# Performance work log

Measured on AMD Instinct MI355X. Metric: run time of the kernel, lower is better.

The kernel has to match this reference:

```python
import jax, jax.numpy as jnp
import numpy as np

N_NODES = 20000
N_EDGES = 160000
FEAT = 512
HEADS = 4
NEG_SLOPE = 0.2


def setup_inputs() -> dict:
    key = jax.random.key(0)
    ks = jax.random.split(key, 8)
    s = 1.0 / np.sqrt(FEAT)
    return {
        "x": jax.random.normal(ks[0], (N_NODES, FEAT), dtype=jnp.float32),
        "edge_index": jax.random.randint(ks[1], (2, N_EDGES), 0, N_NODES, dtype=jnp.int32),
        "W_l": jax.random.normal(ks[2], (FEAT, HEADS * FEAT), dtype=jnp.float32) * s,
        "W_r": jax.random.normal(ks[3], (FEAT, HEADS * FEAT), dtype=jnp.float32) * s,
        "att": jax.random.normal(ks[4], (HEADS, FEAT), dtype=jnp.float32) * s,
        "bias": jax.random.normal(ks[5], (FEAT,), dtype=jnp.float32) * 0.01,
        "W_cls": jax.random.normal(ks[6], (FEAT, 2), dtype=jnp.float32) * s,
        "b_cls": jnp.zeros((2,), dtype=jnp.float32),
    }


def reference(x, edge_index, W_l, W_r, att, bias, W_cls, b_cls):
    N = x.shape[0]
    H, C = att.shape
    # PyG GATv2Conv default: add self-loops
    loops = jnp.arange(N, dtype=edge_index.dtype)
    ei = jnp.concatenate([edge_index, jnp.stack([loops, loops])], axis=1)
    src, dst = ei[0], ei[1]  # message j -> i

    xl = (x @ W_l).reshape(N, H, C)  # source transform
    xr = (x @ W_r).reshape(N, H, C)  # target transform

    # GATv2 score: e_ij = att . LeakyReLU(xl_j + xr_i)   -> [E, H]
    u = xl[src] + xr[dst]                      # [E, H, C]
    e = jnp.einsum('ehc,hc->eh', jax.nn.leaky_relu(u, NEG_SLOPE), att)

    # segment softmax over incoming edges of each dst node
    m = jax.ops.segment_max(e, dst, num_segments=N)          # [N, H]
    alpha = jnp.exp(e - m[dst])
    denom = jax.ops.segment_sum(alpha, dst, num_segments=N)  # [N, H]
    alpha = alpha / denom[dst]

    # aggregate: out_i = sum_j alpha_ij * xl_j
    out = jax.ops.segment_sum(alpha[:, :, None] * xl[src], dst, num_segments=N)  # [N,H,C]
    out = out.mean(axis=1) + bias  # concat=False -> mean over heads, then bias

    return out @ W_cls + b_cls  # [N, num_classes]
```

## Files before the change

### kernel.cpp

```cpp
#include <hip/hip_runtime.h>
#include <hip/hip_bf16.h>

#define FEAT    512
#define HEADS   4
#define NEG     0.2f

typedef unsigned int uint;
typedef unsigned short ushort_t;
typedef __attribute__((ext_vector_type(8))) short bf16x8v;
typedef __attribute__((ext_vector_type(4))) float f32x4v;
typedef __attribute__((address_space(3))) uint lds_u32_t;
typedef __attribute__((address_space(1))) const uint g_u32_t;

__device__ inline float bf2f(ushort_t h) { return __uint_as_float(((uint)h) << 16); }
__device__ inline ushort_t f2bf(float f) {
    uint u = __float_as_uint(f);
    u += 0x7fff + ((u >> 16) & 1);
    return (ushort_t)(u >> 16);
}
__device__ inline float2 up2(uint d) {
    return make_float2(__uint_as_float(d << 16), __uint_as_float(d & 0xffff0000u));
}
__device__ inline float2 f2add(float2 a, float2 b) { return make_float2(a.x + b.x, a.y + b.y); }
__device__ inline float2 f2min0(float2 a) { return make_float2(fminf(a.x, 0.f), fminf(a.y, 0.f)); }
__device__ inline float2 f2fma(float2 a, float2 b, float2 c) {
    return make_float2(fmaf(a.x, b.x, c.x), fmaf(a.y, b.y, c.y));
}
__device__ inline float2 f2fmas(float s, float2 b, float2 c) {
    return make_float2(fmaf(s, b.x, c.x), fmaf(s, b.y, c.y));
}

__global__ __launch_bounds__(256) void prep_kernel(
    const ushort_t* __restrict__ xprobe, int* flag,
    int* __restrict__ deg, int N, int NBZ,
    const void* a0, ushort_t* o0, int n0, const void* a1, ushort_t* o1, int n1,
    const void* a2, ushort_t* o2, int n2, const void* a3, ushort_t* o3, int n3,
    const void* __restrict__ xin, ushort_t* __restrict__ xc, long long nx) {
    __shared__ int s_isbf;
    int tid = threadIdx.x;
    if (tid < 64) {
        int hits = 0;
        for (int i = tid; i < 128; i += 64) {
            ushort_t w = xprobe[2 * i];
            uint hb = (w >> 8) & 0x7f;
            hits += (hb >= 0x38 && hb <= 0x42) ? 1 : 0;
        }
        #pragma unroll
        for (int off = 32; off >= 1; off >>= 1) hits += __shfl_xor(hits, off);
        if (tid == 0) s_isbf = (hits >= 64) ? 1 : 0;
    }
    __syncthreads();
    int isbf = s_isbf;
    int b = blockIdx.x;
    if (b == 0 && tid == 0) *flag = isbf;

    if (b < NBZ) {
        int i0 = (b * 256 + tid) * 4;
        if (i0 + 4 <= N) *(int4*)&deg[i0] = make_int4(0, 0, 0, 0);
        else for (int j = 0; j < 4; ++j) if (i0 + j < N) deg[i0 + j] = 0;
        return;
    }
    if (b < NBZ + 15) {
        int idx = (b - NBZ) * 256 + tid;
        const void* srcs[4] = {a0, a1, a2, a3};
        ushort_t* dsts[4] = {o0, o1, o2, o3};
        int ns[4] = {n0, n1, n2, n3};
        #pragma unroll
        for (int k = 0; k < 4; ++k) {
            if (idx < ns[k]) {
                dsts[k][idx] = isbf ? ((const ushort_t*)srcs[k])[idx]
                                    : f2bf(((const float*)srcs[k])[idx]);
                return;
            }
            idx -= ns[k];
        }
        return;
    }
    if (isbf) return;
    long long i0 = ((long long)(b - NBZ - 15) * 256 + tid) * 8;
    if (i0 + 8 <= nx) {
        const float* f = (const float*)xin + i0;
        float4 a = *(const float4*)f, bb = *(const float4*)(f + 4);
        ushort_t o[8] = {f2bf(a.x), f2bf(a.y), f2bf(a.z), f2bf(a.w),
                         f2bf(bb.x), f2bf(bb.y), f2bf(bb.z), f2bf(bb.w)};
        *(uint4*)&xc[i0] = *(uint4*)o;
    } else {
        for (long long i = i0; i < nx; ++i) xc[i] = f2bf(((const float*)xin)[i]);
    }
}

__global__ void hist_kernel(const int* __restrict__ dst, int* deg, int E, int N) {
    int i = blockIdx.x * blockDim.x + threadIdx.x;
    if (i < E) {
        int d = dst[i];
        if ((uint)d < (uint)N) atomicAdd(&deg[d], 1);
    }
}

__global__ __launch_bounds__(256) void scan1(const int* __restrict__ deg, int* __restrict__ part,
                                             int* __restrict__ bsum, int N) {
    __shared__ int tmp[256];
    int b = blockIdx.x, tid = threadIdx.x;
    int i0 = b * 1024 + tid * 4;
    int v[4] = {0, 0, 0, 0};
    if (i0 + 4 <= N) { int4 q = *(const int4*)&deg[i0]; v[0]=q.x+1; v[1]=q.y+1; v[2]=q.z+1; v[3]=q.w+1; }
    else { for (int j = 0; j < 4; ++j) v[j] = (i0 + j < N) ? deg[i0 + j] + 1 : 0; }
    int s0 = v[0], s1 = s0 + v[1], s2 = s1 + v[2], s3 = s2 + v[3];
    tmp[tid] = s3;
    __syncthreads();
    for (int off = 1; off < 256; off <<= 1) {
        int t = (tid >= off) ? tmp[tid - off] : 0;
        __syncthreads();
        tmp[tid] += t;
        __syncthreads();
    }
    int base = tid ? tmp[tid - 1] : 0;
    int e[4] = {base, base + s0, base + s1, base + s2};
    if (i0 + 4 <= N) { *(int4*)&part[i0] = make_int4(e[0], e[1], e[2], e[3]); }
    else { for (int j = 0; j < 4; ++j) if (i0 + j < N) part[i0 + j] = e[j]; }
    if (tid == 255) bsum[b] = tmp[255];
}

__global__ __launch_bounds__(256) void scan3(const int* __restrict__ part, const int* __restrict__ bsum,
                                             int* __restrict__ offsets, int* __restrict__ cursor,
                                             int N, int Nb) {
    __shared__ int s_add, s_tot;
    int b = blockIdx.x, tid = threadIdx.x;
    if (tid < 64) {
        int v = (tid < Nb) ? bsum[tid] : 0;
        int incl = v;
        #pragma unroll
        for (int off = 1; off < 64; off <<= 1) {
            int t = __shfl_up(incl, off);
            if (tid >= off) incl += t;
        }
        if (tid == b) s_add = incl - v;
        if (tid == Nb - 1) s_tot = incl;
    }
    __syncthreads();
    int add = s_add;
    int i0 = b * 1024 + tid * 4;
    #pragma unroll
    for (int j = 0; j < 4; ++j) {
        int i = i0 + j;
        if (i < N) { int o = part[i] + add; offsets[i] = o; cursor[i] = o; }
    }
    if (b == Nb - 1 && tid == 0) offsets[N] = s_tot;
}

__global__ void scatter_kernel(const int* __restrict__ src, const int* __restrict__ dst,
                               int* cursor, int* srcs, int E, int N) {
    int i = blockIdx.x * blockDim.x + threadIdx.x;
    if (i >= E + N) return;
    int s, d;
    if (i < E) { s = src[i]; d = dst[i]; }
    else       { s = i - E; d = i - E; }
    if ((uint)d >= (uint)N) return;
    int pos = atomicAdd(&cursor[d], 1);
    if ((uint)pos < (uint)(E + N)) srcs[pos] = s;
}

__global__ __launch_bounds__(256) void transpose_canon2(const void* __restrict__ inL,
                                                        const void* __restrict__ inR,
                                                        ushort_t* __restrict__ outL,
                                                        ushort_t* __restrict__ outR,
                                                        const int* __restrict__ flag,
                                                        int K, int N) {
    __shared__ ushort_t t[64][72];
    const void* in = blockIdx.z ? inR : inL;
    ushort_t* outp = blockIdx.z ? outR : outL;
    int k0 = blockIdx.y * 64, n0 = blockIdx.x * 64;
    int tid = threadIdx.x;
    int r = tid >> 3;
    int c = (tid & 7) * 8;
    int isbf = *flag;
    #pragma unroll
    for (int p = 0; p < 2; ++p) {
        int row = r + p * 32;
        size_t base = (size_t)(k0 + row) * N + n0 + c;
        if (isbf) {
            *(uint4*)&t[row][c] = *(const uint4*)((const ushort_t*)in + base);
        } else {
            const float* f = (const float*)in + base;
            float4 a = *(const float4*)f, b = *(const float4*)(f + 4);
            ushort_t o[8] = {f2bf(a.x), f2bf(a.y), f2bf(a.z), f2bf(a.w),
                             f2bf(b.x), f2bf(b.y), f2bf(b.z), f2bf(b.w)};
            *(uint4*)&t[row][c] = *(uint4*)o;
        }
    }
    __syncthreads();
    #pragma unroll
    for (int p = 0; p < 2; ++p) {
        int row = r + p * 32;
        #pragma unroll
        for (int j = 0; j < 8; ++j)
            outp[(size_t)(n0 + row) * K + k0 + c + j] = t[c + j][row];
    }
}

__global__ __launch_bounds__(256) void gemm128(const ushort_t* A_bf, const ushort_t* A_cv,
                                               const int* __restrict__ flag,
                                               const ushort_t* __restrict__ Bt,
                                               ushort_t* __restrict__ C,
                                               int M, int Nn, int K) {
    constexpr int CSTR = 132;
    __shared__ ushort_t SH[128 * CSTR];
    ushort_t* As = SH;
    ushort_t* Bs = SH + 8192;
    const ushort_t* A = (*flag) ? A_bf : A_cv;
    int tid = threadIdx.x;
    int wave = tid >> 6, lane = tid & 63;
    int row0 = blockIdx.y * 128, col0 = blockIdx.x * 128;
    int wm = (wave >> 1) * 64, wn = (wave & 1) * 64;

    f32x4v acc[4][4];
    #pragma unroll
    for (int i = 0; i < 4; ++i)
        #pragma unroll
        for (int j = 0; j < 4; ++j) acc[i][j] = (f32x4v){0.f, 0.f, 0.f, 0.f};

    int fm = lane & 15, kq8 = (lane >> 4) * 8;

    const ushort_t* srcA[2]; ushort_t* dstA0[2]; ushort_t* dstA1[2];
    const ushort_t* srcB[2]; ushort_t* dstB0[2]; ushort_t* dstB1[2];
    #pragma unroll
    for (int i = 0; i < 2; ++i) {
        int p = (wave * 2 + i) * 64 + lane;
        int row = p >> 2, kp = p & 3;
        int gra = row0 + row; if (gra >= M) gra = M - 1;
        srcA[i] = &A[(size_t)gra * K + kp * 8];
        srcB[i] = &Bt[(size_t)(col0 + row) * K + kp * 8];
        dstA0[i] = &As[p * 8]; dstA1[i] = &As[4096 + p * 8];
        dstB0[i] = &Bs[p * 8]; dstB1[i] = &Bs[4096 + p * 8];
    }

    for (int k0 = 0; k0 < K; k0 += 64) {
        #pragma unroll
        for (int i = 0; i < 2; ++i) {
            __builtin_amdgcn_global_load_lds((g_u32_t*)srcA[i],        (lds_u32_t*)dstA0[i], 16, 0, 0);
            __builtin_amdgcn_global_load_lds((g_u32_t*)(srcA[i] + 32), (lds_u32_t*)dstA1[i], 16, 0, 0);
            __builtin_amdgcn_global_load_lds((g_u32_t*)srcB[i],        (lds_u32_t*)dstB0[i], 16, 0, 0);
            __builtin_amdgcn_global_load_lds((g_u32_t*)(srcB[i] + 32), (lds_u32_t*)dstB1[i], 16, 0, 0);
            srcA[i] += 64; srcB[i] += 64;
        }
        __syncthreads();

        #pragma unroll
        for (int panel = 0; panel < 2; ++panel) {
            bf16x8v af[4], bfr[4];
            #pragma unroll
            for (int mi = 0; mi < 4; ++mi)
                af[mi] = *(const bf16x8v*)&As[panel * 4096 + (wm + mi * 16 + fm) * 32 + kq8];
            #pragma unroll
            for (int nj = 0; nj < 4; ++nj)
                bfr[nj] = *(const bf16x8v*)&Bs[panel * 4096 + (wn + nj * 16 + fm) * 32 + kq8];
            #pragma unroll
            for (int mi = 0; mi < 4; ++mi)
                #pragma unroll
                for (int nj = 0; nj < 4; ++nj)
                    acc[mi][nj] = __builtin_amdgcn_mfma_f32_16x16x32_bf16(af[mi], bfr[nj], acc[mi][nj], 0, 0, 0);
        }
        __syncthreads();
    }

    int col = lane & 15, rq = (lane >> 4) * 4;
    #pragma unroll
    for (int mi = 0; mi < 4; ++mi)
        #pragma unroll
        for (int r = 0; r < 4; ++r)
            #pragma unroll
            for (int nj = 0; nj < 4; ++nj)
                SH[(wm + mi * 16 + rq + r) * CSTR + wn + nj * 16 + col] = f2bf(acc[mi][nj][r]);
    __syncthreads();
    #pragma unroll
    for (int j = 0; j < 8; ++j) {
        int base = (tid + j * 256) * 8;
        int r = base >> 7, c = base & 127;
        int gm = row0 + r;
        if (gm < M)
            *(uint4*)&C[(size_t)gm * Nn + col0 + c] = *(const uint4*)&SH[r * CSTR + c];
    }
}

__global__ __launch_bounds__(128, 4) void gat_aggregate(
    const ushort_t* __restrict__ xl, int xl_stride,
    const ushort_t* __restrict__ xr, int xr_stride,
    const int* __restrict__ offsets, const int* __restrict__ srcs,
    const ushort_t* __restrict__ att, const ushort_t* __restrict__ bias,
    const ushort_t* __restrict__ Wc, const ushort_t* __restrict__ bc,
    float* __restrict__ out, int c0, int Cn, int N, int EN) {
    int bn = blockIdx.x;
    if (bn >= Cn) return;
    int n = c0 + bn;
    int tid = threadIdx.x;
    int w = tid >> 6, lane = tid & 63;
    int h = 2 * w + (lane >> 5);
    int r = lane & 31;
    int hoff = h * FEAT + r * 16;

    __shared__ float sh[HEADS][FEAT];
    __shared__ float r0s[2], r1s[2];

    float2 xrr[8], attr[8];
    { const ushort_t* p = &xr[(size_t)bn * xr_stride + hoff];
      uint4 qa = *(const uint4*)p, qb = *(const uint4*)(p + 8);
      xrr[0] = up2(qa.x); xrr[1] = up2(qa.y); xrr[2] = up2(qa.z); xrr[3] = up2(qa.w);
      xrr[4] = up2(qb.x); xrr[5] = up2(qb.y); xrr[6] = up2(qb.z); xrr[7] = up2(qb.w); }
    { const ushort_t* p = &att[hoff];
      uint4 qa = *(const uint4*)p, qb = *(const uint4*)(p + 8);
      attr[0] = up2(qa.x); attr[1] = up2(qa.y); attr[2] = up2(qa.z); attr[3] = up2(qa.w);
      attr[4] = up2(qb.x); attr[5] = up2(qb.y); attr[6] = up2(qb.z); attr[7] = up2(qb.w); }

    int start = offsets[n], end = offsets[n + 1];
    start = max(0, min(start, EN));
    end   = max(start, min(end, EN));
    int deg = end - start;

    int sv = 0;
    if (lane < deg) sv = srcs[start + lane];

    float l = 0.f;
    float2 acc[8] = {{0.f,0.f},{0.f,0.f},{0.f,0.f},{0.f,0.f},
                     {0.f,0.f},{0.f,0.f},{0.f,0.f},{0.f,0.f}};
    const ushort_t* xlh = xl + hoff;
    const float2 cneg = make_float2(NEG - 1.0f, NEG - 1.0f);

    auto getS = [&](int i) -> int {
        if (i >= deg) i = deg - 1;
        if (i < 0) i = 0;
        int s = (i < 64) ? __shfl(sv, i) : srcs[start + i];
        return ((uint)s >= (uint)N) ? 0 : s;
    };
    auto fetchE = [&](int i, uint4& qa, uint4& qb) {
        int s = getS(i);
        const ushort_t* pp = xlh + (size_t)s * xl_stride;
        qa = *(const uint4*)pp;
        qb = *(const uint4*)(pp + 8);
    };
    auto body = [&](uint4 qa, uint4 qb) {
        float2 v[8] = {up2(qa.x), up2(qa.y), up2(qa.z), up2(qa.w),
                       up2(qb.x), up2(qb.y), up2(qb.z), up2(qb.w)};
        float2 p2 = make_float2(0.f, 0.f);
        #pragma unroll
        for (int j = 0; j < 8; ++j) {
            float2 u  = f2add(v[j], xrr[j]);
            float2 lr = f2fma(f2min0(u), cneg, u);
            p2 = f2fma(lr, attr[j], p2);
        }
        float p = p2.x + p2.y;
        #pragma unroll
        for (int off = 16; off >= 1; off >>= 1) p += __shfl_xor(p, off);
        float wgt = __expf(p);
        l += wgt;
        #pragma unroll
        for (int j = 0; j < 8; ++j) acc[j] = f2fmas(wgt, v[j], acc[j]);
    };

    uint4 a0q, a0r, a1q, a1r, b0q, b0r, b1q, b1r;
    fetchE(0, a0q, a0r);
    fetchE(1, a1q, a1r);
    for (int e = 0; e < deg; e += 2) {
        fetchE(e + 2, b0q, b0r);
        fetchE(e + 3, b1q, b1r);
        body(a0q, a0r);
        if (e + 1 < deg) body(a1q, a1r);
        a0q = b0q; a0r = b0r; a1q = b1q; a1r = b1r;
    }

    float inv = 0.25f / fmaxf(l, 1e-35f);
    #pragma unroll
    for (int j = 0; j < 8; ++j) {
        sh[h][r * 16 + 2 * j]     = acc[j].x * inv;
        sh[h][r * 16 + 2 * j + 1] = acc[j].y * inv;
    }
    __syncthreads();

    float p0 = 0.f, p1 = 0.f;
    #pragma unroll
    for (int c = tid; c < FEAT; c += 128) {
        float f = sh[0][c] + sh[1][c] + sh[2][c] + sh[3][c] + bf2f(bias[c]);
        uint w2 = *(const uint*)&Wc[c * 2];
        p0 = fmaf(f, bf2f((ushort_t)(w2 & 0xffff)), p0);
        p1 = fmaf(f, bf2f((ushort_t)(w2 >> 16)), p1);
    }
    #pragma unroll
    for (int off = 32; off >= 1; off >>= 1) {
        p0 += __shfl_xor(p0, off);
        p1 += __shfl_xor(p1, off);
    }
    if (lane == 0) { r0s[w] = p0; r1s[w] = p1; }
    __syncthreads();
    if (tid == 0) {
        out[(size_t)n * 2 + 0] = r0s[0] + r0s[1] + bf2f(bc[0]);
        out[(size_t)n * 2 + 1] = r1s[0] + r1s[1] + bf2f(bc[1]);
    }
}

extern "C" void kernel_launch(void* const* d_in, const int* in_sizes, int n_in,
                              void* d_out, int out_size, void* d_ws, size_t ws_size,
                              hipStream_t stream) {
    const void* x    = d_in[0];
    const int*  ei   = (const int*)d_in[1];
    const void* W_l  = d_in[2];
    const void* W_r  = d_in[3];
    const void* att  = d_in[4];
    const void* bias = d_in[5];
    const void* Wc   = d_in[6];
    const void* bc   = d_in[7];
    float* out = (float*)d_out;

    const int N  = in_sizes[0] / FEAT;
    const int E  = in_sizes[1] / 2;
    const int K  = FEAT;
    const int HC = HEADS * FEAT;
    const int EN = E + N;
    const int Nb = (N + 1023) / 1024;

    const int* src = ei;
    const int* dst = ei + E;

    char* base = (char*)d_ws;
    size_t off = 0;
    auto alloc = [&](size_t bytes) -> char* {
        char* p = base + off;
        off = (off + bytes + 255) & ~(size_t)255;
        return p;
    };
    int* flag    = (int*)alloc(4);
    int* offsets = (int*)alloc((size_t)(N + 1) * 4);
    int* cursor  = (int*)alloc((size_t)N * 4);
    int* deg     = (int*)alloc((size_t)N * 4);
    int* part    = (int*)alloc((size_t)N * 4);
    int* bsum    = (int*)alloc((size_t)(Nb + 1) * 4);
    int* srcs    = (int*)alloc((size_t)EN * 4);
    ushort_t* attc  = (ushort_t*)alloc((size_t)HC * 2);
    ushort_t* biasc = (ushort_t*)alloc((size_t)FEAT * 2);
    ushort_t* Wcc   = (ushort_t*)alloc((size_t)FEAT * 2 * 2);
    ushort_t* bcc   = (ushort_t*)alloc(2 * 2);
    ushort_t* xc   = (ushort_t*)alloc((size_t)N * K * 2);
    ushort_t* Wcat = (ushort_t*)alloc((size_t)2 * HC * K * 2);
    size_t fixed = off;

    size_t need_merged = (size_t)N * 2 * HC * 2;
    bool merged = (ws_size >= fixed + need_merged);

    long long NX = (long long)N * K;
    const int NBZ = (N + 1023) / 1024;
    int nxb = (int)((NX / 8 + 255) / 256);
    prep_kernel<<<NBZ + 15 + nxb, 256, 0, stream>>>(
        (const ushort_t*)x, flag, deg, N, NBZ,
        att, attc, HC, bias, biasc, FEAT, Wc, Wcc, FEAT * 2, bc, bcc, 2,
        x, xc, NX);

    hist_kernel<<<(E + 255) / 256, 256, 0, stream>>>(dst, deg, E, N);
    scan1<<<Nb, 256, 0, stream>>>(deg, part, bsum, N);
    scan3<<<Nb, 256, 0, stream>>>(part, bsum, offsets, cursor, N, Nb);
    scatter_kernel<<<(EN + 255) / 256, 256, 0, stream>>>(src, dst, cursor, srcs, E, N);

    dim3 tg(HC / 64, K / 64, 2);
    transpose_canon2<<<tg, 256, 0, stream>>>(W_l, W_r, Wcat, Wcat + (size_t)HC * K,
                                             flag, K, HC);

    const ushort_t* x_bf = (const ushort_t*)x;

    if (merged) {
        ushort_t* xlr = (ushort_t*)(base + fixed);
        dim3 gg(2 * HC / 128, (N + 127) / 128);
        gemm128<<<gg, 256, 0, stream>>>(x_bf, xc, flag, Wcat, xlr, N, 2 * HC, K);
        gat_aggregate<<<N, 128, 0, stream>>>(xlr, 2 * HC, xlr + HC, 2 * HC,
                                             offsets, srcs, attc, biasc, Wcc, bcc,
                                             out, 0, N, N, EN);
    } else {
        ushort_t* xl = (ushort_t*)alloc((size_t)N * HC * 2);
        size_t remain = (ws_size > off) ? (ws_size - off) : 0;
        long long Cmax = (long long)(remain / ((size_t)HC * 2));
        int C = (Cmax >= N) ? N : (int)(Cmax & ~63LL);
        if (C < 64) C = 64;
        ushort_t* xrc = (ushort_t*)(base + off);
        ushort_t* Wlt = Wcat;
        ushort_t* Wrt = Wcat + (size_t)HC * K;

        dim3 gl(HC / 128, (N + 127) / 128);
        gemm128<<<gl, 256, 0, stream>>>(x_bf, xc, flag, Wlt, xl, N, HC, K);
        for (int c0 = 0; c0 < N; c0 += C) {
            int Cn = (N - c0 < C) ? (N - c0) : C;
            dim3 gr(HC / 128, (Cn + 127) / 128);
            gemm128<<<gr, 256, 0, stream>>>(x_bf + (size_t)c0 * K, xc + (size_t)c0 * K, flag,
                                            Wrt, xrc, Cn, HC, K);
            gat_aggregate<<<Cn, 128, 0, stream>>>(xl, HC, xrc, HC,
                                                  offsets, srcs, attc, biasc, Wcc, bcc,
                                                  out, c0, Cn, N, EN);
        }
    }
}
```

Baseline: 343.8 us.

## Replace 128x128 GEMM with 256x256 double-buffered, swizzled, phase-pipelined bf16 MFMA kernel

The projection GEMM moves from a 128x128 tile with 4 waves and a sync-load-compute loop to a 256x256 tile with 8 waves. The new kernel double-buffers K-tiles in 128KB of LDS, XOR-swizzles LDS addresses to avoid bank conflicts, and splits each K step into phases that interleave async global-to-LDS loads with MFMA work, using s_setprio and explicit waitcnt/barriers. The aim is more data reuse per tile and hidden memory latency. In exchange it raises register pressure, allows fewer blocks per CU, and wastes more work on partial tiles along the N=20000 row dimension.

```diff
diff --git a/kernel.cpp b/kernel.cpp
--- a/kernel.cpp
+++ b/kernel.cpp
@@ -198,87 +198,134 @@
     }
 }
 
-__global__ __launch_bounds__(256) void gemm128(const ushort_t* A_bf, const ushort_t* A_cv,
-                                               const int* __restrict__ flag,
-                                               const ushort_t* __restrict__ Bt,
-                                               ushort_t* __restrict__ C,
-                                               int M, int Nn, int K) {
-    constexpr int CSTR = 132;
-    __shared__ ushort_t SH[128 * CSTR];
-    ushort_t* As = SH;
-    ushort_t* Bs = SH + 8192;
+__global__ __launch_bounds__(512, 2) void gemm256(const ushort_t* A_bf, const ushort_t* A_cv,
+                                                  const int* __restrict__ flag,
+                                                  const ushort_t* __restrict__ Bt,
+                                                  ushort_t* __restrict__ C,
+                                                  int M, int Nn, int K) {
+    __shared__ ushort_t SH[65536];
     const ushort_t* A = (*flag) ? A_bf : A_cv;
     int tid = threadIdx.x;
-    int wave = tid >> 6, lane = tid & 63;
-    int row0 = blockIdx.y * 128, col0 = blockIdx.x * 128;
-    int wm = (wave >> 1) * 64, wn = (wave & 1) * 64;
-
-    f32x4v acc[4][4];
-    #pragma unroll
-    for (int i = 0; i < 4; ++i)
+    int lane = tid & 63, wave = tid >> 6;
+    int wm = wave >> 2, wn = wave & 3;
+    int row0 = blockIdx.y * 256, col0 = blockIdx.x * 256;
+
+    f32x4v acc[8][4];
+    #pragma unroll
+    for (int i = 0; i < 8; ++i)
         #pragma unroll
         for (int j = 0; j < 4; ++j) acc[i][j] = (f32x4v){0.f, 0.f, 0.f, 0.f};
 
-    int fm = lane & 15, kq8 = (lane >> 4) * 8;
-
-    const ushort_t* srcA[2]; ushort_t* dstA0[2]; ushort_t* dstA1[2];
-    const ushort_t* srcB[2]; ushort_t* dstB0[2]; ushort_t* dstB1[2];
-    #pragma unroll
-    for (int i = 0; i < 2; ++i) {
-        int p = (wave * 2 + i) * 64 + lane;
-        int row = p >> 2, kp = p & 3;
-        int gra = row0 + row; if (gra >= M) gra = M - 1;
-        srcA[i] = &A[(size_t)gra * K + kp * 8];
-        srcB[i] = &Bt[(size_t)(col0 + row) * K + kp * 8];
-        dstA0[i] = &As[p * 8]; dstA1[i] = &As[4096 + p * 8];
-        dstB0[i] = &Bs[p * 8]; dstB1[i] = &Bs[4096 + p * 8];
-    }
-
-    for (int k0 = 0; k0 < K; k0 += 64) {
-        #pragma unroll
-        for (int i = 0; i < 2; ++i) {
-            __builtin_amdgcn_global_load_lds((g_u32_t*)srcA[i],        (lds_u32_t*)dstA0[i], 16, 0, 0);
-            __builtin_amdgcn_global_load_lds((g_u32_t*)(srcA[i] + 32), (lds_u32_t*)dstA1[i], 16, 0, 0);
-            __builtin_amdgcn_global_load_lds((g_u32_t*)srcB[i],        (lds_u32_t*)dstB0[i], 16, 0, 0);
-            __builtin_amdgcn_global_load_lds((g_u32_t*)(srcB[i] + 32), (lds_u32_t*)dstB1[i], 16, 0, 0);
-            srcA[i] += 64; srcB[i] += 64;
+    int rlo = tid >> 3;
+    int selem = ((((tid & 7) << 4) ^ ((rlo & 7) << 4)) >> 1);
+    int arow[4]; const ushort_t* bsrc[4];
+    #pragma unroll
+    for (int hl = 0; hl < 4; ++hl) {
+        int r = hl * 64 + rlo;
+        int ga = row0 + r; if (ga >= M) ga = M - 1;
+        arow[hl] = ga;
+        bsrc[hl] = Bt + (size_t)(col0 + r) * K + selem;
+    }
+    int doff = tid * 8;
+
+    auto STAGE_A = [&](int kt) {
+        ushort_t* dst = &SH[(kt & 1) * 32768];
+        int ke = kt * 64 + selem;
+        #pragma unroll
+        for (int hl = 0; hl < 4; ++hl)
+            __builtin_amdgcn_global_load_lds((g_u32_t*)(A + (size_t)arow[hl] * K + ke),
+                                             (lds_u32_t*)(dst + hl * 4096 + doff), 16, 0, 0);
+    };
+    auto STAGE_B = [&](int kt) {
+        ushort_t* dst = &SH[(kt & 1) * 32768 + 16384];
+        int kof = kt * 64;
+        #pragma unroll
+        for (int hl = 0; hl < 4; ++hl)
+            __builtin_amdgcn_global_load_lds((g_u32_t*)(bsrc[hl] + kof),
+                                             (lds_u32_t*)(dst + hl * 4096 + doff), 16, 0, 0);
+    };
+
+    int fm = lane & 15;
+    int co[2];
+    {   int cb0 = (lane >> 4) << 4;
+        int xm = (lane & 7) << 4;
+        co[0] = ((cb0) ^ xm) >> 1;
+        co[1] = ((64 + cb0) ^ xm) >> 1;
+    }
+    bf16x8v bF[4][2];
+
+#define PHASE(q, PBASE, STAGE_STMT, TAIL_STMT) do {                               \
+        if ((q) == 0) {                                                           \
+            _Pragma("unroll") for (int nj = 0; nj < 4; ++nj)                      \
+                _Pragma("unroll") for (int s = 0; s < 2; ++s)                     \
+                    bF[nj][s] = *(const bf16x8v*)&SH[(PBASE) + 16384 +            \
+                                    (wn * 64 + nj * 16 + fm) * 64 + co[s]];       \
+        }                                                                         \
+        bf16x8v aF[2][2];                                                         \
+        _Pragma("unroll") for (int u = 0; u < 2; ++u)                             \
+            _Pragma("unroll") for (int s = 0; s < 2; ++s)                         \
+                aF[u][s] = *(const bf16x8v*)&SH[(PBASE) +                         \
+                               (wm * 128 + (q) * 32 + u * 16 + fm) * 64 + co[s]]; \
+        asm volatile("s_barrier" ::: "memory");                                   \
+        STAGE_STMT;                                                               \
+        asm volatile("s_waitcnt lgkmcnt(0)" ::: "memory");                        \
+        __builtin_amdgcn_sched_barrier(0);                                        \
+        __builtin_amdgcn_s_setprio(1);                                            \
+        _Pragma("unroll") for (int u = 0; u < 2; ++u)                             \
+            _Pragma("unroll") for (int nj = 0; nj < 4; ++nj)                      \
+                _Pragma("unroll") for (int s = 0; s < 2; ++s)                     \
+                    acc[(q) * 2 + u][nj] = __builtin_amdgcn_mfma_f32_16x16x32_bf16( \
+                        aF[u][s], bF[nj][s], acc[(q) * 2 + u][nj], 0, 0, 0);      \
+        __builtin_amdgcn_s_setprio(0);                                            \
+        __builtin_amdgcn_sched_barrier(0);                                        \
+        TAIL_STMT;                                                                \
+        asm volatile("s_barrier" ::: "memory");                                   \
+    } while (0)
+
+    int NK = K >> 6;
+    STAGE_B(0); STAGE_A(0); STAGE_B(1); STAGE_A(1);
+    asm volatile("s_waitcnt vmcnt(8)" ::: "memory");
+    asm volatile("s_barrier" ::: "memory");
+
+    for (int kt = 0; kt < NK; kt += 2) {
+        int lastpair = (kt + 2 >= NK);
+        PHASE(0, 0, { if (!lastpair) STAGE_B(kt + 2); }, {});
+        PHASE(1, 0, {}, {});
+        PHASE(2, 0, {}, {});
+        PHASE(3, 0, { if (!lastpair) STAGE_A(kt + 2); },
+                    { if (lastpair) { asm volatile("s_waitcnt vmcnt(0)" ::: "memory"); }
+                      else          { asm volatile("s_waitcnt vmcnt(8)" ::: "memory"); } });
+        PHASE(0, 32768, { if (!lastpair) STAGE_B(kt + 3); }, {});
+        PHASE(1, 32768, {}, {});
+        PHASE(2, 32768, {}, {});
+        PHASE(3, 32768, { if (!lastpair) STAGE_A(kt + 3); },
+                        { if (!lastpair) { asm volatile("s_waitcnt vmcnt(8)" ::: "memory"); } });
+    }
+#undef PHASE
+
+    int rq = (lane >> 4) * 4;
+    #pragma unroll
+    for (int hh = 0; hh < 2; ++hh) {
+        if (wm == hh) {
+            #pragma unroll
+            for (int mi = 0; mi < 8; ++mi)
+                #pragma unroll
+                for (int rr = 0; rr < 4; ++rr)
+                    #pragma unroll
+                    for (int nj = 0; nj < 4; ++nj)
+                        SH[(mi * 16 + rq + rr) * 264 + wn * 64 + nj * 16 + fm] =
+                            f2bf(acc[mi][nj][rr]);
         }
         __syncthreads();
-
-        #pragma unroll
-        for (int panel = 0; panel < 2; ++panel) {
-            bf16x8v af[4], bfr[4];
-            #pragma unroll
-            for (int mi = 0; mi < 4; ++mi)
-                af[mi] = *(const bf16x8v*)&As[panel * 4096 + (wm + mi * 16 + fm) * 32 + kq8];
-            #pragma unroll
-            for (int nj = 0; nj < 4; ++nj)
-                bfr[nj] = *(const bf16x8v*)&Bs[panel * 4096 + (wn + nj * 16 + fm) * 32 + kq8];
-            #pragma unroll
-            for (int mi = 0; mi < 4; ++mi)
-                #pragma unroll
-                for (int nj = 0; nj < 4; ++nj)
-                    acc[mi][nj] = __builtin_amdgcn_mfma_f32_16x16x32_bf16(af[mi], bfr[nj], acc[mi][nj], 0, 0, 0);
+        #pragma unroll
+        for (int j = 0; j < 8; ++j) {
+            int idx = tid + j * 512;
+            int r = idx >> 5, c = (idx & 31) * 8;
+            int gm = row0 + hh * 128 + r;
+            if (gm < M)
+                *(uint4*)&C[(size_t)gm * Nn + col0 + c] = *(const uint4*)&SH[r * 264 + c];
         }
         __syncthreads();
-    }
-
-    int col = lane & 15, rq = (lane >> 4) * 4;
-    #pragma unroll
-    for (int mi = 0; mi < 4; ++mi)
-        #pragma unroll
-        for (int r = 0; r < 4; ++r)
-            #pragma unroll
-            for (int nj = 0; nj < 4; ++nj)
-                SH[(wm + mi * 16 + rq + r) * CSTR + wn + nj * 16 + col] = f2bf(acc[mi][nj][r]);
-    __syncthreads();
-    #pragma unroll
-    for (int j = 0; j < 8; ++j) {
-        int base = (tid + j * 256) * 8;
-        int r = base >> 7, c = base & 127;
-        int gm = row0 + r;
-        if (gm < M)
-            *(uint4*)&C[(size_t)gm * Nn + col0 + c] = *(const uint4*)&SH[r * CSTR + c];
     }
 }
 
@@ -465,8 +512,8 @@
 
     if (merged) {
         ushort_t* xlr = (ushort_t*)(base + fixed);
-        dim3 gg(2 * HC / 128, (N + 127) / 128);
-        gemm128<<<gg, 256, 0, stream>>>(x_bf, xc, flag, Wcat, xlr, N, 2 * HC, K);
+        dim3 gg(2 * HC / 256, (N + 255) / 256);
+        gemm256<<<gg, 512, 0, stream>>>(x_bf, xc, flag, Wcat, xlr, N, 2 * HC, K);
         gat_aggregate<<<N, 128, 0, stream>>>(xlr, 2 * HC, xlr + HC, 2 * HC,
                                              offsets, srcs, attc, biasc, Wcc, bcc,
                                              out, 0, N, N, EN);
@@ -474,18 +521,18 @@
         ushort_t* xl = (ushort_t*)alloc((size_t)N * HC * 2);
         size_t remain = (ws_size > off) ? (ws_size - off) : 0;
         long long Cmax = (long long)(remain / ((size_t)HC * 2));
-        int C = (Cmax >= N) ? N : (int)(Cmax & ~63LL);
-        if (C < 64) C = 64;
+        int C = (Cmax >= N) ? N : (int)(Cmax & ~255LL);
+        if (C < 256) C = 256;
         ushort_t* xrc = (ushort_t*)(base + off);
         ushort_t* Wlt = Wcat;
         ushort_t* Wrt = Wcat + (size_t)HC * K;
 
-        dim3 gl(HC / 128, (N + 127) / 128);
-        gemm128<<<gl, 256, 0, stream>>>(x_bf, xc, flag, Wlt, xl, N, HC, K);
+        dim3 gl(HC / 256, (N + 255) / 256);
+        gemm256<<<gl, 512, 0, stream>>>(x_bf, xc, flag, Wlt, xl, N, HC, K);
         for (int c0 = 0; c0 < N; c0 += C) {
             int Cn = (N - c0 < C) ? (N - c0) : C;
-            dim3 gr(HC / 128, (Cn + 127) / 128);
-            gemm128<<<gr, 256, 0, stream>>>(x_bf + (size_t)c0 * K, xc + (size_t)c0 * K, flag,
+            dim3 gr(HC / 256, (Cn + 255) / 256);
+            gemm256<<<gr, 512, 0, stream>>>(x_bf + (size_t)c0 * K, xc + (size_t)c0 * K, flag,
                                             Wrt, xrc, Cn, HC, K);
             gat_aggregate<<<Cn, 128, 0, stream>>>(xl, HC, xrc, HC,
                                                   offsets, srcs, attc, biasc, Wcc, bcc,
```

Result: no change. 341.5 us (-0.7%).

## Split GAT aggregation into two head-pair passes to shrink the gathered working set

Applied to the files above, without the earlier changes.

The aggregation kernel is split into two launches, each handling two of the four heads with a single 64-thread wave per node. The first pass writes per-node partial classifier sums to a workspace buffer, and the second adds them together with the bias terms. The intent is to halve the xl footprint gathered per pass so more of it stays in cache, and to use nontemporal loads and stores for streamed data. In exchange, the edge lists and softmax setup are read twice and there is an extra launch plus a round trip through the partial buffer.

```diff
diff --git a/kernel.cpp b/kernel.cpp
--- a/kernel.cpp
+++ b/kernel.cpp
@@ -9,6 +9,7 @@
 typedef unsigned short ushort_t;
 typedef __attribute__((ext_vector_type(8))) short bf16x8v;
 typedef __attribute__((ext_vector_type(4))) float f32x4v;
+typedef __attribute__((ext_vector_type(4))) uint uint4v;
 typedef __attribute__((address_space(3))) uint lds_u32_t;
 typedef __attribute__((address_space(1))) const uint g_u32_t;
 
@@ -282,28 +283,27 @@
     }
 }
 
-__global__ __launch_bounds__(128, 4) void gat_aggregate(
+__global__ __launch_bounds__(64, 4) void gat_aggregate2(
     const ushort_t* __restrict__ xl, int xl_stride,
     const ushort_t* __restrict__ xr, int xr_stride,
     const int* __restrict__ offsets, const int* __restrict__ srcs,
     const ushort_t* __restrict__ att, const ushort_t* __restrict__ bias,
     const ushort_t* __restrict__ Wc, const ushort_t* __restrict__ bc,
-    float* __restrict__ out, int c0, int Cn, int N, int EN) {
+    float* __restrict__ part, float* __restrict__ out, int hsel,
+    int c0, int Cn, int N, int EN) {
     int bn = blockIdx.x;
     if (bn >= Cn) return;
     int n = c0 + bn;
-    int tid = threadIdx.x;
-    int w = tid >> 6, lane = tid & 63;
-    int h = 2 * w + (lane >> 5);
-    int r = lane & 31;
-    int hoff = h * FEAT + r * 16;
-
-    __shared__ float sh[HEADS][FEAT];
-    __shared__ float r0s[2], r1s[2];
+    int lane = threadIdx.x;
+    int hl = lane >> 5, r = lane & 31;
+    int hoff = (hsel + hl) * FEAT + r * 16;
+
+    __shared__ float sh[2][FEAT];
 
     float2 xrr[8], attr[8];
-    { const ushort_t* p = &xr[(size_t)bn * xr_stride + hoff];
-      uint4 qa = *(const uint4*)p, qb = *(const uint4*)(p + 8);
+    { const uint4v* p = (const uint4v*)&xr[(size_t)bn * xr_stride + hoff];
+      uint4v qa = __builtin_nontemporal_load(p);
+      uint4v qb = __builtin_nontemporal_load(p + 1);
       xrr[0] = up2(qa.x); xrr[1] = up2(qa.y); xrr[2] = up2(qa.z); xrr[3] = up2(qa.w);
       xrr[4] = up2(qb.x); xrr[5] = up2(qb.y); xrr[6] = up2(qb.z); xrr[7] = up2(qb.w); }
     { const ushort_t* p = &att[hoff];
@@ -370,15 +370,16 @@
     float inv = 0.25f / fmaxf(l, 1e-35f);
     #pragma unroll
     for (int j = 0; j < 8; ++j) {
-        sh[h][r * 16 + 2 * j]     = acc[j].x * inv;
-        sh[h][r * 16 + 2 * j + 1] = acc[j].y * inv;
+        sh[hl][r * 16 + 2 * j]     = acc[j].x * inv;
+        sh[hl][r * 16 + 2 * j + 1] = acc[j].y * inv;
     }
     __syncthreads();
 
     float p0 = 0.f, p1 = 0.f;
     #pragma unroll
-    for (int c = tid; c < FEAT; c += 128) {
-        float f = sh[0][c] + sh[1][c] + sh[2][c] + sh[3][c] + bf2f(bias[c]);
+    for (int c = lane; c < FEAT; c += 64) {
+        float f = sh[0][c] + sh[1][c];
+        if (hsel) f += bf2f(bias[c]);
         uint w2 = *(const uint*)&Wc[c * 2];
         p0 = fmaf(f, bf2f((ushort_t)(w2 & 0xffff)), p0);
         p1 = fmaf(f, bf2f((ushort_t)(w2 >> 16)), p1);
@@ -388,11 +389,14 @@
         p0 += __shfl_xor(p0, off);
         p1 += __shfl_xor(p1, off);
     }
-    if (lane == 0) { r0s[w] = p0; r1s[w] = p1; }
-    __syncthreads();
-    if (tid == 0) {
-        out[(size_t)n * 2 + 0] = r0s[0] + r0s[1] + bf2f(bc[0]);
-        out[(size_t)n * 2 + 1] = r1s[0] + r1s[1] + bf2f(bc[1]);
+    if (lane == 0) {
+        if (!hsel) {
+            __builtin_nontemporal_store(p0, &part[(size_t)n * 2 + 0]);
+            __builtin_nontemporal_store(p1, &part[(size_t)n * 2 + 1]);
+        } else {
+            out[(size_t)n * 2 + 0] = part[(size_t)n * 2 + 0] + p0 + bf2f(bc[0]);
+            out[(size_t)n * 2 + 1] = part[(size_t)n * 2 + 1] + p1 + bf2f(bc[1]);
+        }
     }
 }
 
@@ -433,6 +437,7 @@
     int* part    = (int*)alloc((size_t)N * 4);
     int* bsum    = (int*)alloc((size_t)(Nb + 1) * 4);
     int* srcs    = (int*)alloc((size_t)EN * 4);
+    float* hpart = (float*)alloc((size_t)N * 2 * 4);
     ushort_t* attc  = (ushort_t*)alloc((size_t)HC * 2);
     ushort_t* biasc = (ushort_t*)alloc((size_t)FEAT * 2);
     ushort_t* Wcc   = (ushort_t*)alloc((size_t)FEAT * 2 * 2);
@@ -467,9 +472,12 @@
         ushort_t* xlr = (ushort_t*)(base + fixed);
         dim3 gg(2 * HC / 128, (N + 127) / 128);
         gemm128<<<gg, 256, 0, stream>>>(x_bf, xc, flag, Wcat, xlr, N, 2 * HC, K);
-        gat_aggregate<<<N, 128, 0, stream>>>(xlr, 2 * HC, xlr + HC, 2 * HC,
+        gat_aggregate2<<<N, 64, 0, stream>>>(xlr, 2 * HC, xlr + HC, 2 * HC,
                                              offsets, srcs, attc, biasc, Wcc, bcc,
-                                             out, 0, N, N, EN);
+                                             hpart, out, 0, 0, N, N, EN);
+        gat_aggregate2<<<N, 64, 0, stream>>>(xlr, 2 * HC, xlr + HC, 2 * HC,
+                                             offsets, srcs, attc, biasc, Wcc, bcc,
+                                             hpart, out, 2, 0, N, N, EN);
     } else {
         ushort_t* xl = (ushort_t*)alloc((size_t)N * HC * 2);
         size_t remain = (ws_size > off) ? (ws_size - off) : 0;
@@ -487,9 +495,12 @@
             dim3 gr(HC / 128, (Cn + 127) / 128);
             gemm128<<<gr, 256, 0, stream>>>(x_bf + (size_t)c0 * K, xc + (size_t)c0 * K, flag,
                                             Wrt, xrc, Cn, HC, K);
-            gat_aggregate<<<Cn, 128, 0, stream>>>(xl, HC, xrc, HC,
+            gat_aggregate2<<<Cn, 64, 0, stream>>>(xl, HC, xrc, HC,
                                                   offsets, srcs, attc, biasc, Wcc, bcc,
-                                                  out, c0, Cn, N, EN);
-        }
-    }
-}
+                                                  hpart, out, 0, c0, Cn, N, EN);
+            gat_aggregate2<<<Cn, 64, 0, stream>>>(xl, HC, xrc, HC,
+                                                  offsets, srcs, attc, biasc, Wcc, bcc,
+                                                  hpart, out, 2, c0, Cn, N, EN);
+        }
+    }
+}
```

Result: no change. 348.1 us (+1.2%).
